# Kernel tuning notes

Hardware: AMD Instinct MI355X
Metric: run time of the kernel (lower is better)

Reference implementation:

```python
import jax, jax.numpy as jnp
import numpy as np

B, S, HID, HEADS = 8, 1024, 1024, 16
DK = HID // HEADS


def setup_inputs() -> dict:
    key = jax.random.key(0)
    ks = jax.random.split(key, 6)
    scale = 1.0 / np.sqrt(HID)
    return {
        "q": jax.random.normal(ks[0], (B, S, HID), jnp.float32),
        "k": jax.random.normal(ks[1], (B, S, HID), jnp.float32),
        "v": jax.random.normal(ks[2], (B, S, HID), jnp.float32),
        "Wq": jax.random.normal(ks[3], (HID, HID), jnp.float32) * scale,
        "Wk": jax.random.normal(ks[4], (HID, HID), jnp.float32) * scale,
        "Wv": jax.random.normal(ks[5], (HID, HID), jnp.float32) * scale,
        "mask": 1,
    }


def _split_heads(x):
    # [B, S, HID] -> [B, HEADS, S, DK]
    b, s, _ = x.shape
    return x.reshape(b, s, HEADS, DK).transpose(0, 2, 1, 3)


def reference(q, k, v, Wq, Wk, Wv, mask):
    # torch nn.Linear: y = x @ W.T (no bias)
    qh = _split_heads(q @ Wq.T)
    kh = _split_heads(k @ Wk.T)
    vh = _split_heads(v @ Wv.T)

    scores = jnp.einsum("bhqd,bhkd->bhqk", qh, kh) / jnp.sqrt(jnp.asarray(DK, qh.dtype))
    scores = jax.nn.softmax(scores, axis=-1)
    if mask:
        # original zeroes entries where row > col AFTER softmax (keeps upper triangle)
        tri = jnp.triu(jnp.ones((S, S), scores.dtype))
        scores = scores * tri
        # original then transposes the (masked) score matrix before applying to V
        scores = scores.transpose(0, 1, 3, 2)
    out = jnp.einsum("bhqk,bhkd->bhqd", scores, vh)
    # [B, HEADS, S, DK] -> [B, S, HID]
    return out.transpose(0, 2, 1, 3).reshape(q.shape[0], -1, HID)
```

## Files before the change

### kernel.cpp

```cpp
#include <hip/hip_runtime.h>
#include <math.h>

#define B 8
#define S 1024
#define HID 1024
#define HEADS 16
#define DK 64

typedef unsigned short u16;
typedef unsigned int u32;
typedef _Float16 f16;
typedef __attribute__((ext_vector_type(8))) _Float16 half8;
typedef __attribute__((ext_vector_type(4))) _Float16 half4;
typedef __attribute__((ext_vector_type(2))) _Float16 half2;
typedef __attribute__((ext_vector_type(2))) __fp16 fp16x2;
typedef __attribute__((ext_vector_type(4))) float f32x4;

#define GLL16(G, L)                                                         \
    __builtin_amdgcn_global_load_lds(                                       \
        (const __attribute__((address_space(1))) u32*)(G),                  \
        (__attribute__((address_space(3))) u32*)(L), 16, 0, 0)

__device__ __forceinline__ float exp_s(float c) {
#if __has_builtin(__builtin_amdgcn_exp2f)
    return __builtin_amdgcn_exp2f(c);
#else
    return exp2f(c);
#endif
}

__global__ __launch_bounds__(256) void cast_all(
    const float* __restrict__ q, const float* __restrict__ k,
    const float* __restrict__ v, const float* __restrict__ Wq,
    const float* __restrict__ Wk, const float* __restrict__ Wv,
    f16* __restrict__ oq, f16* __restrict__ ok, f16* __restrict__ ov,
    f16* __restrict__ owq, f16* __restrict__ owk, f16* __restrict__ owv) {
    const size_t SZ = (size_t)B * S * HID;
    const size_t WZ = (size_t)HID * HID;
    size_t e = ((size_t)blockIdx.x * 256 + threadIdx.x) * 8;
    const float* src;
    f16* dst;
    if (e < SZ)               { src = q + e;               dst = oq + e; }
    else if (e < 2 * SZ)      { src = k + (e - SZ);        dst = ok + (e - SZ); }
    else if (e < 3 * SZ)      { src = v + (e - 2 * SZ);    dst = ov + (e - 2 * SZ); }
    else if (e < 3 * SZ + WZ) { src = Wq + (e - 3 * SZ);   dst = owq + (e - 3 * SZ); }
    else if (e < 3 * SZ + 2 * WZ) { src = Wk + (e - 3 * SZ - WZ); dst = owk + (e - 3 * SZ - WZ); }
    else                      { src = Wv + (e - 3 * SZ - 2 * WZ); dst = owv + (e - 3 * SZ - 2 * WZ); }
    f32x4 a = *(const f32x4*)src;
    f32x4 b = *(const f32x4*)(src + 4);
    half8 h;
    h[0] = (f16)a[0]; h[1] = (f16)a[1]; h[2] = (f16)a[2]; h[3] = (f16)a[3];
    h[4] = (f16)b[0]; h[5] = (f16)b[1]; h[6] = (f16)b[2]; h[7] = (f16)b[3];
    *(half8*)dst = h;
}

__global__ __launch_bounds__(256) void proj_mfma_b(
    const f16* __restrict__ Xq, const f16* __restrict__ Xk,
    const f16* __restrict__ Xv, const f16* __restrict__ Wq,
    const f16* __restrict__ Wk, const f16* __restrict__ Wv,
    f16* __restrict__ Qb, f16* __restrict__ Kb, f16* __restrict__ Vt) {
    const int L = blockIdx.x;
    const int xcd = L & 7;
    const int w8 = L >> 3;
    const int cx = w8 & 7;
    const int g = xcd * 24 + (w8 >> 3);
    const int z = g % 3;
    const int ytile = g / 3;

    const f16* __restrict__ X = (z == 0) ? Xq : (z == 1) ? Xk : Xv;
    const f16* __restrict__ W = (z == 0) ? Wq : (z == 1) ? Wk : Wv;

    __shared__ u16 As[128 * 32];
    __shared__ u16 Bs[128 * 32];
    const int tid = threadIdx.x;
    const int wv = tid >> 6, ln = tid & 63;
    const int lr = ln & 15, quad = ln >> 4;
    const int wm = wv >> 1, wn = wv & 1;
    const int row0 = ytile * 128, col0 = cx * 128;

    const int srow = tid >> 2;
    const int sch = tid & 3;

    f32x4 acc[4][4];
    #pragma unroll
    for (int i = 0; i < 4; ++i)
        #pragma unroll
        for (int j = 0; j < 4; ++j) acc[i][j] = (f32x4){0.f, 0.f, 0.f, 0.f};

    for (int k0 = 0; k0 < HID; k0 += 32) {
        #pragma unroll
        for (int p = 0; p < 2; ++p) {
            int r = p * 64 + srow;
            int csw = sch ^ ((r >> 1) & 3);
            GLL16(X + (size_t)(row0 + r) * HID + k0 + csw * 8, As + p * 2048 + tid * 8);
            GLL16(W + (size_t)(col0 + r) * HID + k0 + csw * 8, Bs + p * 2048 + tid * 8);
        }
        __syncthreads();
        half8 a[4], b[4];
        #pragma unroll
        for (int mi = 0; mi < 4; ++mi) {
            int r = wm * 64 + mi * 16 + lr;
            a[mi] = *(const half8*)(As + r * 32 + ((quad ^ ((r >> 1) & 3)) * 8));
        }
        #pragma unroll
        for (int ni = 0; ni < 4; ++ni) {
            int r = wn * 64 + ni * 16 + lr;
            b[ni] = *(const half8*)(Bs + r * 32 + ((quad ^ ((r >> 1) & 3)) * 8));
        }
        #pragma unroll
        for (int mi = 0; mi < 4; ++mi)
            #pragma unroll
            for (int ni = 0; ni < 4; ++ni)
                acc[mi][ni] = __builtin_amdgcn_mfma_f32_16x16x32_f16(
                    a[mi], b[ni], acc[mi][ni], 0, 0, 0);
        __syncthreads();
    }

    if (z < 2) {
        f16* __restrict__ Y = (z == 0) ? Qb : Kb;
        const float sc = (z == 0) ? 0.18033688f : 1.0f;
        #pragma unroll
        for (int mi = 0; mi < 4; ++mi) {
            int m = row0 + wm * 64 + mi * 16 + quad * 4;
            #pragma unroll
            for (int ni = 0; ni < 4; ++ni) {
                int n = col0 + wn * 64 + ni * 16 + lr;
                #pragma unroll
                for (int r = 0; r < 4; ++r)
                    Y[(size_t)(m + r) * HID + n] = (f16)(acc[mi][ni][r] * sc);
            }
        }
    } else {
        #pragma unroll
        for (int mi = 0; mi < 4; ++mi) {
            int m = row0 + wm * 64 + mi * 16 + quad * 4;
            int bb = m >> 10, s = m & 1023;
            #pragma unroll
            for (int ni = 0; ni < 4; ++ni) {
                int n = col0 + wn * 64 + ni * 16 + lr;
                half4 h4;
                #pragma unroll
                for (int r = 0; r < 4; ++r) h4[r] = (f16)acc[mi][ni][r];
                *(half4*)(Vt + ((size_t)(bb * 16 + (n >> 6)) * 64 + (n & 63)) * S + s) = h4;
            }
        }
    }
}

__global__ __launch_bounds__(256) void stats_mfma(const f16* __restrict__ Q,
                                                  const f16* __restrict__ K,
                                                  f16* __restrict__ Vt) {
    const int bh = blockIdx.x, jt = blockIdx.y;
    const int b = bh >> 4, h = bh & 15;
    const int tid = threadIdx.x;
    const int wv = tid >> 6, ln = tid & 63;
    const int lr = ln & 15, quad = ln >> 4;
    __shared__ u16 Ks[2][64 * 64];
    __shared__ float rlL[128];

    auto stageK = [&](int bufi, int i0v) {
        #pragma unroll
        for (int p = 0; p < 2; ++p) {
            int r = p * 32 + (tid >> 3);
            int csw = (tid & 7) ^ (r & 7);
            GLL16(K + (size_t)(b * S + i0v + r) * HID + h * 64 + csw * 8,
                  Ks[bufi] + p * 2048 + tid * 8);
        }
    };

    stageK(0, 0);

    half8 aq[2][2];
    #pragma unroll
    for (int jsub = 0; jsub < 2; ++jsub) {
        const int j = jt * 128 + wv * 32 + jsub * 16 + lr;
        const f16* qrow = Q + (size_t)(b * S + j) * HID + h * 64;
        aq[jsub][0] = *(const half8*)(qrow + quad * 8);
        aq[jsub][1] = *(const half8*)(qrow + 32 + quad * 8);
    }

    float sl[2][4] = {};

    for (int t = 0; t < S / 64; ++t) {
        __syncthreads();
        if (t + 1 < S / 64) stageK((t + 1) & 1, (t + 1) * 64);
        const u16* Kst = Ks[t & 1];
        #pragma unroll
        for (int isub = 0; isub < 4; ++isub) {
            int il = isub * 16 + lr;
            half8 bk0 = *(const half8*)(Kst + il * 64 + (((0 + quad) ^ (il & 7)) * 8));
            half8 bk1 = *(const half8*)(Kst + il * 64 + (((4 + quad) ^ (il & 7)) * 8));
            #pragma unroll
            for (int jsub = 0; jsub < 2; ++jsub) {
                f32x4 c = {0.f, 0.f, 0.f, 0.f};
                c = __builtin_amdgcn_mfma_f32_16x16x32_f16(aq[jsub][0], bk0, c, 0, 0, 0);
                c = __builtin_amdgcn_mfma_f32_16x16x32_f16(aq[jsub][1], bk1, c, 0, 0, 0);
                #pragma unroll
                for (int r = 0; r < 4; ++r) sl[jsub][r] += exp_s(c[r]);
            }
        }
    }

    #pragma unroll
    for (int jsub = 0; jsub < 2; ++jsub)
        #pragma unroll
        for (int r = 0; r < 4; ++r) {
            float v = sl[jsub][r];
            v += __shfl_xor(v, 1, 64);
            v += __shfl_xor(v, 2, 64);
            v += __shfl_xor(v, 4, 64);
            v += __shfl_xor(v, 8, 64);
            if (lr == 0) rlL[wv * 32 + jsub * 16 + quad * 4 + r] = 1.0f / v;
        }
    __syncthreads();

    {
        const int d = tid >> 2, lc = (tid & 3) * 8;
        f16* vrow = Vt + (size_t)(bh * 64 + d) * S + jt * 128;
        #pragma unroll
        for (int g = 0; g < 4; ++g) {
            const int c0 = g * 32 + lc;
            half8 hv = *(half8*)(vrow + c0);
            #pragma unroll
            for (int e = 0; e < 8; ++e)
                hv[e] = (f16)((float)hv[e] * rlL[c0 + e]);
            *(half8*)(vrow + c0) = hv;
        }
    }
}

__global__ __launch_bounds__(256) void apply_mfma(const f16* __restrict__ Q,
                                                  const f16* __restrict__ K,
                                                  const f16* __restrict__ Vt,
                                                  float* __restrict__ out) {
    const int bh = blockIdx.x;
    const int it2 = (gridDim.y - 1) - blockIdx.y;
    const int b = bh >> 4, h = bh & 15;
    const int tid = threadIdx.x;
    const int wv = tid >> 6, ln = tid & 63;
    const int lr = ln & 15, quad = ln >> 4;
    const int i0b = it2 * 128;
    const int i0w = i0b + wv * 32;

    __shared__ u16 Qs[2][64 * 64];
    __shared__ u16 Vts[2][64 * 64];

    auto stageQV = [&](int bufi, int j0v) {
        #pragma unroll
        for (int p = 0; p < 2; ++p) {
            int r = p * 32 + (tid >> 3);
            int csw = (tid & 7) ^ (r & 7);
            GLL16(Q + (size_t)(b * S + j0v + r) * HID + h * 64 + csw * 8,
                  Qs[bufi] + p * 2048 + tid * 8);
        }
        #pragma unroll
        for (int p = 0; p < 2; ++p) {
            int d = p * 32 + (tid >> 3);
            int csw = (tid & 7) ^ (d & 7);
            GLL16(Vt + (size_t)(bh * 64 + d) * S + j0v + csw * 8,
                  Vts[bufi] + p * 2048 + tid * 8);
        }
    };

    stageQV(0, 0);

    half8 bk[2][2];
    #pragma unroll
    for (int isub = 0; isub < 2; ++isub) {
        int i = i0w + isub * 16 + lr;
        #pragma unroll
        for (int kf = 0; kf < 2; ++kf)
            bk[isub][kf] = *(const half8*)(K + (size_t)(b * S + i) * HID + h * 64 +
                                           kf * 32 + quad * 8);
    }

    f32x4 acc[4][2];
    #pragma unroll
    for (int nt = 0; nt < 4; ++nt)
        #pragma unroll
        for (int isub = 0; isub < 2; ++isub) acc[nt][isub] = (f32x4){0.f, 0.f, 0.f, 0.f};

    const int nch = 2 * it2 + 2;
    for (int jc = 0; jc < nch; ++jc) {
        const int j0 = jc * 64;
        __syncthreads();
        if (jc + 1 < nch) stageQV((jc + 1) & 1, j0 + 64);
        const u16* Qsc = Qs[jc & 1];
        const u16* Vsc = Vts[jc & 1];

        #pragma unroll
        for (int jsub = 0; jsub < 4; ++jsub) {
            const int jbase = j0 + jsub * 16;
            if (jbase > i0w + 31) break;

            const int jl = jsub * 16 + lr;
            half8 aq0 = *(const half8*)(Qsc + jl * 64 + (((0 + quad) ^ (jl & 7)) * 8));
            half8 aq1 = *(const half8*)(Qsc + jl * 64 + (((4 + quad) ^ (jl & 7)) * 8));
            half4 av[4];
            #pragma unroll
            for (int nt = 0; nt < 4; ++nt) {
                int d = nt * 16 + lr;
                int ch = (jsub * 2 + (quad >> 1)) ^ (d & 7);
                av[nt] = *(const half4*)(Vsc + d * 64 + ch * 8 + (quad & 1) * 4);
            }

            #pragma unroll
            for (int isub = 0; isub < 2; ++isub) {
                const int ib = i0w + isub * 16;
                if (jbase > ib + 15) continue;
                f32x4 c = {0.f, 0.f, 0.f, 0.f};
                c = __builtin_amdgcn_mfma_f32_16x16x32_f16(aq0, bk[isub][0], c, 0, 0, 0);
                c = __builtin_amdgcn_mfma_f32_16x16x32_f16(aq1, bk[isub][1], c, 0, 0, 0);
                float w0 = exp_s(c[0]), w1 = exp_s(c[1]);
                float w2 = exp_s(c[2]), w3 = exp_s(c[3]);
                if (jbase + 15 > ib) {
                    const int i_col = ib + lr;
                    const int jq = jbase + quad * 4;
                    if (jq + 0 > i_col) w0 = 0.f;
                    if (jq + 1 > i_col) w1 = 0.f;
                    if (jq + 2 > i_col) w2 = 0.f;
                    if (jq + 3 > i_col) w3 = 0.f;
                }
                fp16x2 q0 = __builtin_amdgcn_cvt_pkrtz(w0, w1);
                fp16x2 q1 = __builtin_amdgcn_cvt_pkrtz(w2, w3);
                half2 p0 = __builtin_bit_cast(half2, q0);
                half2 p1 = __builtin_bit_cast(half2, q1);
                half4 bw;
                bw[0] = p0[0]; bw[1] = p0[1]; bw[2] = p1[0]; bw[3] = p1[1];
                #pragma unroll
                for (int nt = 0; nt < 4; ++nt)
                    acc[nt][isub] = __builtin_amdgcn_mfma_f32_16x16x16f16(
                        av[nt], bw, acc[nt][isub], 0, 0, 0);
            }
        }
    }

    #pragma unroll
    for (int isub = 0; isub < 2; ++isub) {
        int i = i0w + isub * 16 + lr;
        #pragma unroll
        for (int nt = 0; nt < 4; ++nt)
            *(f32x4*)(out + (size_t)(b * S + i) * HID + h * 64 + nt * 16 + quad * 4) =
                acc[nt][isub];
    }
}

extern "C" void kernel_launch(void* const* d_in, const int* in_sizes, int n_in,
                              void* d_out, int out_size, void* d_ws, size_t ws_size,
                              hipStream_t stream) {
    const float* q  = (const float*)d_in[0];
    const float* k  = (const float*)d_in[1];
    const float* v  = (const float*)d_in[2];
    const float* Wq = (const float*)d_in[3];
    const float* Wk = (const float*)d_in[4];
    const float* Wv = (const float*)d_in[5];

    const size_t SZ = (size_t)B * S * HID;
    const size_t WZ = (size_t)HID * HID;

    f16* xq = (f16*)d_out;
    f16* xk = xq + SZ;

    char* p = (char*)d_ws;
    f16* xv = (f16*)p;      p += SZ * 2;
    f16* wq = (f16*)p;      p += WZ * 2;
    f16* wk = (f16*)p;      p += WZ * 2;
    f16* wv_ = (f16*)p;     p += WZ * 2;
    f16* Qb = (f16*)p;      p += SZ * 2;
    f16* Kb = (f16*)p;      p += SZ * 2;
    f16* Vt = (f16*)p;      p += SZ * 2;

    float* out = (float*)d_out;

    const int ncast = (int)((3 * SZ + 3 * WZ) / 8 / 256);
    cast_all<<<ncast, 256, 0, stream>>>(q, k, v, Wq, Wk, Wv,
                                        xq, xk, xv, wq, wk, wv_);

    proj_mfma_b<<<1536, 256, 0, stream>>>(xq, xk, xv, wq, wk, wv_, Qb, Kb, Vt);

    stats_mfma<<<dim3(B * HEADS, S / 128), 256, 0, stream>>>(Qb, Kb, Vt);
    apply_mfma<<<dim3(B * HEADS, S / 128), 256, 0, stream>>>(Qb, Kb, Vt, out);
}
```

Measured before the change: 285.3 us.

## Rework projection GEMM into triple-buffered 256x128 tile pipeline with 8 waves

The Q/K/V projection kernel moves from a 128x128 tile with a single-stage K=32 loop to a 256x128 tile with 512 threads and a K=64 step. Three LDS buffers let global-to-LDS loads for later K steps run while the current step computes, with explicit vmcnt and lgkmcnt waits. Barriers and s_setprio interleave LDS reads with MFMA bursts, and the workgroup-to-XCD mapping changes. The aim is to hide load latency and raise MFMA utilization. In exchange the kernel uses about 144KB of LDS, which limits it to one block per CU, and depends on hand-written wait counts being correct.

```diff
diff --git a/kernel.cpp b/kernel.cpp
--- a/kernel.cpp
+++ b/kernel.cpp
@@ -20,6 +20,8 @@
     __builtin_amdgcn_global_load_lds(                                       \
         (const __attribute__((address_space(1))) u32*)(G),                  \
         (__attribute__((address_space(3))) u32*)(L), 16, 0, 0)
+
+#define MF32(a, b, c) __builtin_amdgcn_mfma_f32_16x16x32_f16((a), (b), (c), 0, 0, 0)
 
 __device__ __forceinline__ float exp_s(float c) {
 #if __has_builtin(__builtin_amdgcn_exp2f)
@@ -54,32 +56,47 @@
     *(half8*)dst = h;
 }
 
-__global__ __launch_bounds__(256) void proj_mfma_b(
+__global__ __launch_bounds__(512, 2) void proj_mfma_b(
     const f16* __restrict__ Xq, const f16* __restrict__ Xk,
     const f16* __restrict__ Xv, const f16* __restrict__ Wq,
     const f16* __restrict__ Wk, const f16* __restrict__ Wv,
     f16* __restrict__ Qb, f16* __restrict__ Kb, f16* __restrict__ Vt) {
     const int L = blockIdx.x;
-    const int xcd = L & 7;
-    const int w8 = L >> 3;
-    const int cx = w8 & 7;
-    const int g = xcd * 24 + (w8 >> 3);
-    const int z = g % 3;
-    const int ytile = g / 3;
+    const int wg = (L & 7) * 96 + (L >> 3);
+    const int z = wg >> 8;
+    const int rm = wg & 255;
+    const int ytile = rm >> 3;
+    const int cx = rm & 7;
 
     const f16* __restrict__ X = (z == 0) ? Xq : (z == 1) ? Xk : Xv;
     const f16* __restrict__ W = (z == 0) ? Wq : (z == 1) ? Wk : Wv;
-
-    __shared__ u16 As[128 * 32];
-    __shared__ u16 Bs[128 * 32];
+    const int row0 = ytile * 256, col0 = cx * 128;
+
+    __shared__ u16 As[3][256 * 64];
+    __shared__ u16 Bs[3][128 * 64];
+
     const int tid = threadIdx.x;
     const int wv = tid >> 6, ln = tid & 63;
     const int lr = ln & 15, quad = ln >> 4;
     const int wm = wv >> 1, wn = wv & 1;
-    const int row0 = ytile * 128, col0 = cx * 128;
-
-    const int srow = tid >> 2;
-    const int sch = tid & 3;
+    const int rr = tid >> 3, ch = tid & 7;
+
+    auto stage = [&](int kt, int bi) {
+        const f16* Xb = X + (size_t)row0 * HID + kt * 64;
+        const f16* Wb = W + (size_t)col0 * HID + kt * 64;
+        #pragma unroll
+        for (int p = 0; p < 4; ++p) {
+            int row = p * 64 + rr;
+            GLL16(Xb + (size_t)row * HID + ((ch ^ (row & 7)) * 8),
+                  &As[bi][p * 4096 + tid * 8]);
+        }
+        #pragma unroll
+        for (int p = 0; p < 2; ++p) {
+            int row = p * 64 + rr;
+            GLL16(Wb + (size_t)row * HID + ((ch ^ (row & 7)) * 8),
+                  &Bs[bi][p * 4096 + tid * 8]);
+        }
+    };
 
     f32x4 acc[4][4];
     #pragma unroll
@@ -87,33 +104,77 @@
         #pragma unroll
         for (int j = 0; j < 4; ++j) acc[i][j] = (f32x4){0.f, 0.f, 0.f, 0.f};
 
-    for (int k0 = 0; k0 < HID; k0 += 32) {
-        #pragma unroll
-        for (int p = 0; p < 2; ++p) {
-            int r = p * 64 + srow;
-            int csw = sch ^ ((r >> 1) & 3);
-            GLL16(X + (size_t)(row0 + r) * HID + k0 + csw * 8, As + p * 2048 + tid * 8);
-            GLL16(W + (size_t)(col0 + r) * HID + k0 + csw * 8, Bs + p * 2048 + tid * 8);
-        }
-        __syncthreads();
-        half8 a[4], b[4];
-        #pragma unroll
-        for (int mi = 0; mi < 4; ++mi) {
-            int r = wm * 64 + mi * 16 + lr;
-            a[mi] = *(const half8*)(As + r * 32 + ((quad ^ ((r >> 1) & 3)) * 8));
-        }
-        #pragma unroll
-        for (int ni = 0; ni < 4; ++ni) {
-            int r = wn * 64 + ni * 16 + lr;
-            b[ni] = *(const half8*)(Bs + r * 32 + ((quad ^ ((r >> 1) & 3)) * 8));
-        }
-        #pragma unroll
-        for (int mi = 0; mi < 4; ++mi)
-            #pragma unroll
-            for (int ni = 0; ni < 4; ++ni)
-                acc[mi][ni] = __builtin_amdgcn_mfma_f32_16x16x32_f16(
-                    a[mi], b[ni], acc[mi][ni], 0, 0, 0);
-        __syncthreads();
+    stage(0, 0);
+    stage(1, 1);
+    asm volatile("s_waitcnt vmcnt(6)" ::: "memory");
+    __builtin_amdgcn_s_barrier();
+
+    int bi = 0, sbi = 2;
+    #pragma unroll
+    for (int u = 0; u < 16; ++u) {
+        const u16* A = As[bi];
+        const u16* Bh = Bs[bi];
+        auto rdA = [&](int mi, int ks) -> half8 {
+            int row = wm * 64 + mi * 16 + lr;
+            int pc = (ks * 4 + quad) ^ (row & 7);
+            return *(const half8*)(A + row * 64 + pc * 8);
+        };
+        auto rdB = [&](int ni, int ks) -> half8 {
+            int row = wn * 64 + ni * 16 + lr;
+            int pc = (ks * 4 + quad) ^ (row & 7);
+            return *(const half8*)(Bh + row * 64 + pc * 8);
+        };
+
+        if (u < 14) stage(u + 2, sbi);
+        half8 a00 = rdA(0, 0), a01 = rdA(0, 1), a10 = rdA(1, 0), a11 = rdA(1, 1);
+        half8 b00 = rdB(0, 0), b01 = rdB(0, 1), b10 = rdB(1, 0), b11 = rdB(1, 1);
+        __builtin_amdgcn_s_barrier();
+        asm volatile("s_waitcnt lgkmcnt(0)" ::: "memory");
+        __builtin_amdgcn_s_setprio(1);
+        acc[0][0] = MF32(a00, b00, acc[0][0]); acc[0][0] = MF32(a01, b01, acc[0][0]);
+        acc[0][1] = MF32(a00, b10, acc[0][1]); acc[0][1] = MF32(a01, b11, acc[0][1]);
+        acc[1][0] = MF32(a10, b00, acc[1][0]); acc[1][0] = MF32(a11, b01, acc[1][0]);
+        acc[1][1] = MF32(a10, b10, acc[1][1]); acc[1][1] = MF32(a11, b11, acc[1][1]);
+        __builtin_amdgcn_s_setprio(0);
+        __builtin_amdgcn_s_barrier();
+
+        half8 b20 = rdB(2, 0), b21 = rdB(2, 1), b30 = rdB(3, 0), b31 = rdB(3, 1);
+        __builtin_amdgcn_s_barrier();
+        asm volatile("s_waitcnt lgkmcnt(0)" ::: "memory");
+        __builtin_amdgcn_s_setprio(1);
+        acc[0][2] = MF32(a00, b20, acc[0][2]); acc[0][2] = MF32(a01, b21, acc[0][2]);
+        acc[0][3] = MF32(a00, b30, acc[0][3]); acc[0][3] = MF32(a01, b31, acc[0][3]);
+        acc[1][2] = MF32(a10, b20, acc[1][2]); acc[1][2] = MF32(a11, b21, acc[1][2]);
+        acc[1][3] = MF32(a10, b30, acc[1][3]); acc[1][3] = MF32(a11, b31, acc[1][3]);
+        __builtin_amdgcn_s_setprio(0);
+        __builtin_amdgcn_s_barrier();
+
+        half8 a20 = rdA(2, 0), a21 = rdA(2, 1), a30 = rdA(3, 0), a31 = rdA(3, 1);
+        __builtin_amdgcn_s_barrier();
+        asm volatile("s_waitcnt lgkmcnt(0)" ::: "memory");
+        __builtin_amdgcn_s_setprio(1);
+        acc[2][2] = MF32(a20, b20, acc[2][2]); acc[2][2] = MF32(a21, b21, acc[2][2]);
+        acc[2][3] = MF32(a20, b30, acc[2][3]); acc[2][3] = MF32(a21, b31, acc[2][3]);
+        acc[3][2] = MF32(a30, b20, acc[3][2]); acc[3][2] = MF32(a31, b21, acc[3][2]);
+        acc[3][3] = MF32(a30, b30, acc[3][3]); acc[3][3] = MF32(a31, b31, acc[3][3]);
+        __builtin_amdgcn_s_setprio(0);
+        __builtin_amdgcn_s_barrier();
+
+        __builtin_amdgcn_s_setprio(1);
+        acc[2][0] = MF32(a20, b00, acc[2][0]); acc[2][0] = MF32(a21, b01, acc[2][0]);
+        acc[2][1] = MF32(a20, b10, acc[2][1]); acc[2][1] = MF32(a21, b11, acc[2][1]);
+        acc[3][0] = MF32(a30, b00, acc[3][0]); acc[3][0] = MF32(a31, b01, acc[3][0]);
+        acc[3][1] = MF32(a30, b10, acc[3][1]); acc[3][1] = MF32(a31, b11, acc[3][1]);
+        __builtin_amdgcn_s_setprio(0);
+        if (u < 14) {
+            asm volatile("s_waitcnt vmcnt(6)" ::: "memory");
+        } else if (u == 14) {
+            asm volatile("s_waitcnt vmcnt(0)" ::: "memory");
+        }
+        __builtin_amdgcn_s_barrier();
+
+        bi = (bi + 1 == 3) ? 0 : bi + 1;
+        sbi = (sbi + 1 == 3) ? 0 : sbi + 1;
     }
 
     if (z < 2) {
@@ -376,7 +437,7 @@
     cast_all<<<ncast, 256, 0, stream>>>(q, k, v, Wq, Wk, Wv,
                                         xq, xk, xv, wq, wk, wv_);
 
-    proj_mfma_b<<<1536, 256, 0, stream>>>(xq, xk, xv, wq, wk, wv_, Qb, Kb, Vt);
+    proj_mfma_b<<<768, 512, 0, stream>>>(xq, xk, xv, wq, wk, wv_, Qb, Kb, Vt);
 
     stats_mfma<<<dim3(B * HEADS, S / 128), 256, 0, stream>>>(Qb, Kb, Vt);
     apply_mfma<<<dim3(B * HEADS, S / 128), 256, 0, stream>>>(Qb, Kb, Vt, out);
```

New measurement: 280.0 us. No clear change (-1.9%).

## Fuse fp32-to-fp16 activation cast into projection GEMM with double-buffered LDS

Applied to the files above, without the earlier changes.

Drops the separate cast pass over q/k/v. The projection kernel now loads fp32 activations into registers, converts them to fp16 and writes them into a swizzled LDS tile. The LDS tiles are double-buffered so the next k-slice loads overlap the current MFMA work, and only the weights are still pre-cast. This saves writing and re-reading 3x fp16 activation copies. In exchange the GEMM reads twice the activation bytes per tile and holds more registers, and each iteration ends with a vmcnt(0) wait.

```diff
diff --git a/kernel.cpp b/kernel.cpp
--- a/kernel.cpp
+++ b/kernel.cpp
@@ -21,6 +21,8 @@
         (const __attribute__((address_space(1))) u32*)(G),                  \
         (__attribute__((address_space(3))) u32*)(L), 16, 0, 0)
 
+#define MF32(a, b, c) __builtin_amdgcn_mfma_f32_16x16x32_f16((a), (b), (c), 0, 0, 0)
+
 __device__ __forceinline__ float exp_s(float c) {
 #if __has_builtin(__builtin_amdgcn_exp2f)
     return __builtin_amdgcn_exp2f(c);
@@ -29,23 +31,17 @@
 #endif
 }
 
-__global__ __launch_bounds__(256) void cast_all(
-    const float* __restrict__ q, const float* __restrict__ k,
-    const float* __restrict__ v, const float* __restrict__ Wq,
-    const float* __restrict__ Wk, const float* __restrict__ Wv,
-    f16* __restrict__ oq, f16* __restrict__ ok, f16* __restrict__ ov,
+__global__ __launch_bounds__(256) void cast_w(
+    const float* __restrict__ Wq, const float* __restrict__ Wk,
+    const float* __restrict__ Wv,
     f16* __restrict__ owq, f16* __restrict__ owk, f16* __restrict__ owv) {
-    const size_t SZ = (size_t)B * S * HID;
     const size_t WZ = (size_t)HID * HID;
     size_t e = ((size_t)blockIdx.x * 256 + threadIdx.x) * 8;
     const float* src;
     f16* dst;
-    if (e < SZ)               { src = q + e;               dst = oq + e; }
-    else if (e < 2 * SZ)      { src = k + (e - SZ);        dst = ok + (e - SZ); }
-    else if (e < 3 * SZ)      { src = v + (e - 2 * SZ);    dst = ov + (e - 2 * SZ); }
-    else if (e < 3 * SZ + WZ) { src = Wq + (e - 3 * SZ);   dst = owq + (e - 3 * SZ); }
-    else if (e < 3 * SZ + 2 * WZ) { src = Wk + (e - 3 * SZ - WZ); dst = owk + (e - 3 * SZ - WZ); }
-    else                      { src = Wv + (e - 3 * SZ - 2 * WZ); dst = owv + (e - 3 * SZ - 2 * WZ); }
+    if (e < WZ)          { src = Wq + e;          dst = owq + e; }
+    else if (e < 2 * WZ) { src = Wk + (e - WZ);   dst = owk + (e - WZ); }
+    else                 { src = Wv + (e - 2*WZ); dst = owv + (e - 2*WZ); }
     f32x4 a = *(const f32x4*)src;
     f32x4 b = *(const f32x4*)(src + 4);
     half8 h;
@@ -55,8 +51,8 @@
 }
 
 __global__ __launch_bounds__(256) void proj_mfma_b(
-    const f16* __restrict__ Xq, const f16* __restrict__ Xk,
-    const f16* __restrict__ Xv, const f16* __restrict__ Wq,
+    const float* __restrict__ Xq, const float* __restrict__ Xk,
+    const float* __restrict__ Xv, const f16* __restrict__ Wq,
     const f16* __restrict__ Wk, const f16* __restrict__ Wv,
     f16* __restrict__ Qb, f16* __restrict__ Kb, f16* __restrict__ Vt) {
     const int L = blockIdx.x;
@@ -67,19 +63,20 @@
     const int z = g % 3;
     const int ytile = g / 3;
 
-    const f16* __restrict__ X = (z == 0) ? Xq : (z == 1) ? Xk : Xv;
+    const float* __restrict__ X = (z == 0) ? Xq : (z == 1) ? Xk : Xv;
     const f16* __restrict__ W = (z == 0) ? Wq : (z == 1) ? Wk : Wv;
 
-    __shared__ u16 As[128 * 32];
-    __shared__ u16 Bs[128 * 32];
+    __shared__ u16 As[2][128 * 32];
+    __shared__ u16 Bs[2][128 * 32];
     const int tid = threadIdx.x;
     const int wv = tid >> 6, ln = tid & 63;
     const int lr = ln & 15, quad = ln >> 4;
     const int wm = wv >> 1, wn = wv & 1;
     const int row0 = ytile * 128, col0 = cx * 128;
 
-    const int srow = tid >> 2;
-    const int sch = tid & 3;
+    const int arow = tid >> 1, ahalf = tid & 1;
+    const float* Xrow = X + (size_t)(row0 + arow) * HID + ahalf * 16;
+    const int brow = tid >> 2, bsch = tid & 3;
 
     f32x4 acc[4][4];
     #pragma unroll
@@ -87,32 +84,65 @@
         #pragma unroll
         for (int j = 0; j < 4; ++j) acc[i][j] = (f32x4){0.f, 0.f, 0.f, 0.f};
 
-    for (int k0 = 0; k0 < HID; k0 += 32) {
+    f32x4 ar[4];
+    auto loadA = [&](int k0) {
+        #pragma unroll
+        for (int j = 0; j < 4; ++j)
+            ar[j] = *(const f32x4*)(Xrow + k0 + j * 4);
+    };
+    auto writeA = [&](int bufi) {
+        half8 h0, h1;
+        h0[0] = (f16)ar[0][0]; h0[1] = (f16)ar[0][1]; h0[2] = (f16)ar[0][2]; h0[3] = (f16)ar[0][3];
+        h0[4] = (f16)ar[1][0]; h0[5] = (f16)ar[1][1]; h0[6] = (f16)ar[1][2]; h0[7] = (f16)ar[1][3];
+        h1[0] = (f16)ar[2][0]; h1[1] = (f16)ar[2][1]; h1[2] = (f16)ar[2][2]; h1[3] = (f16)ar[2][3];
+        h1[4] = (f16)ar[3][0]; h1[5] = (f16)ar[3][1]; h1[6] = (f16)ar[3][2]; h1[7] = (f16)ar[3][3];
+        const int sw = (arow >> 1) & 3;
+        *(half8*)(&As[bufi][arow * 32 + ((ahalf * 2 + 0) ^ sw) * 8]) = h0;
+        *(half8*)(&As[bufi][arow * 32 + ((ahalf * 2 + 1) ^ sw) * 8]) = h1;
+    };
+    auto stageB = [&](int k0, int bufi) {
         #pragma unroll
         for (int p = 0; p < 2; ++p) {
-            int r = p * 64 + srow;
-            int csw = sch ^ ((r >> 1) & 3);
-            GLL16(X + (size_t)(row0 + r) * HID + k0 + csw * 8, As + p * 2048 + tid * 8);
-            GLL16(W + (size_t)(col0 + r) * HID + k0 + csw * 8, Bs + p * 2048 + tid * 8);
-        }
-        __syncthreads();
+            int r = p * 64 + brow;
+            int csw = bsch ^ ((r >> 1) & 3);
+            GLL16(W + (size_t)(col0 + r) * HID + k0 + csw * 8,
+                  &Bs[bufi][p * 2048 + tid * 8]);
+        }
+    };
+
+    loadA(0);
+    stageB(0, 0);
+    asm volatile("s_waitcnt vmcnt(0)" ::: "memory");
+    writeA(0);
+    __syncthreads();
+
+    #pragma unroll 2
+    for (int t = 0; t < 32; ++t) {
+        const int cur = t & 1, nxt = cur ^ 1;
+        if (t < 31) {
+            loadA((t + 1) * 32);
+            stageB((t + 1) * 32, nxt);
+        }
         half8 a[4], b[4];
         #pragma unroll
         for (int mi = 0; mi < 4; ++mi) {
             int r = wm * 64 + mi * 16 + lr;
-            a[mi] = *(const half8*)(As + r * 32 + ((quad ^ ((r >> 1) & 3)) * 8));
+            a[mi] = *(const half8*)(&As[cur][r * 32 + ((quad ^ ((r >> 1) & 3)) * 8)]);
         }
         #pragma unroll
         for (int ni = 0; ni < 4; ++ni) {
             int r = wn * 64 + ni * 16 + lr;
-            b[ni] = *(const half8*)(Bs + r * 32 + ((quad ^ ((r >> 1) & 3)) * 8));
+            b[ni] = *(const half8*)(&Bs[cur][r * 32 + ((quad ^ ((r >> 1) & 3)) * 8)]);
         }
         #pragma unroll
         for (int mi = 0; mi < 4; ++mi)
             #pragma unroll
             for (int ni = 0; ni < 4; ++ni)
-                acc[mi][ni] = __builtin_amdgcn_mfma_f32_16x16x32_f16(
-                    a[mi], b[ni], acc[mi][ni], 0, 0, 0);
+                acc[mi][ni] = MF32(a[mi], b[ni], acc[mi][ni]);
+        if (t < 31) {
+            asm volatile("s_waitcnt vmcnt(0)" ::: "memory");
+            writeA(nxt);
+        }
         __syncthreads();
     }
 
@@ -358,11 +388,7 @@
     const size_t SZ = (size_t)B * S * HID;
     const size_t WZ = (size_t)HID * HID;
 
-    f16* xq = (f16*)d_out;
-    f16* xk = xq + SZ;
-
     char* p = (char*)d_ws;
-    f16* xv = (f16*)p;      p += SZ * 2;
     f16* wq = (f16*)p;      p += WZ * 2;
     f16* wk = (f16*)p;      p += WZ * 2;
     f16* wv_ = (f16*)p;     p += WZ * 2;
@@ -372,11 +398,10 @@
 
     float* out = (float*)d_out;
 
-    const int ncast = (int)((3 * SZ + 3 * WZ) / 8 / 256);
-    cast_all<<<ncast, 256, 0, stream>>>(q, k, v, Wq, Wk, Wv,
-                                        xq, xk, xv, wq, wk, wv_);
-
-    proj_mfma_b<<<1536, 256, 0, stream>>>(xq, xk, xv, wq, wk, wv_, Qb, Kb, Vt);
+    const int ncast = (int)(3 * WZ / 8 / 256);
+    cast_w<<<ncast, 256, 0, stream>>>(Wq, Wk, Wv, wq, wk, wv_);
+
+    proj_mfma_b<<<1536, 256, 0, stream>>>(q, k, v, wq, wk, wv_, Qb, Kb, Vt);
 
     stats_mfma<<<dim3(B * HEADS, S / 128), 256, 0, stream>>>(Qb, Kb, Vt);
     apply_mfma<<<dim3(B * HEADS, S / 128), 256, 0, stream>>>(Qb, Kb, Vt, out);
```

New measurement: 317.1 us. 1.11x slower.

## Replace LDS double-buffered staging with direct global loads in stats and apply kernels

Applied to the files above, without the earlier changes.

Both the stats and apply attention kernels stop staging K, Q and transposed V tiles into shared memory with async global-to-LDS copies and barriers. Each wave now reads its MFMA operands straight from global memory, relying on L1/L2 caching. This removes the __syncthreads barriers and LDS traffic, and lets the apply kernel loop per 16-row chunk with per-wave early exit. The cost is redundant global and cache reads across the four waves, plus exposed load latency with no explicit prefetch.

```diff
diff --git a/kernel.cpp b/kernel.cpp
--- a/kernel.cpp
+++ b/kernel.cpp
@@ -155,20 +155,7 @@
     const int tid = threadIdx.x;
     const int wv = tid >> 6, ln = tid & 63;
     const int lr = ln & 15, quad = ln >> 4;
-    __shared__ u16 Ks[2][64 * 64];
     __shared__ float rlL[128];
-
-    auto stageK = [&](int bufi, int i0v) {
-        #pragma unroll
-        for (int p = 0; p < 2; ++p) {
-            int r = p * 32 + (tid >> 3);
-            int csw = (tid & 7) ^ (r & 7);
-            GLL16(K + (size_t)(b * S + i0v + r) * HID + h * 64 + csw * 8,
-                  Ks[bufi] + p * 2048 + tid * 8);
-        }
-    };
-
-    stageK(0, 0);
 
     half8 aq[2][2];
     #pragma unroll
@@ -181,15 +168,13 @@
 
     float sl[2][4] = {};
 
-    for (int t = 0; t < S / 64; ++t) {
-        __syncthreads();
-        if (t + 1 < S / 64) stageK((t + 1) & 1, (t + 1) * 64);
-        const u16* Kst = Ks[t & 1];
+    for (int i0 = 0; i0 < S; i0 += 64) {
         #pragma unroll
         for (int isub = 0; isub < 4; ++isub) {
-            int il = isub * 16 + lr;
-            half8 bk0 = *(const half8*)(Kst + il * 64 + (((0 + quad) ^ (il & 7)) * 8));
-            half8 bk1 = *(const half8*)(Kst + il * 64 + (((4 + quad) ^ (il & 7)) * 8));
+            const int i = i0 + isub * 16 + lr;
+            const f16* krow = K + (size_t)(b * S + i) * HID + h * 64;
+            half8 bk0 = *(const half8*)(krow + quad * 8);
+            half8 bk1 = *(const half8*)(krow + 32 + quad * 8);
             #pragma unroll
             for (int jsub = 0; jsub < 2; ++jsub) {
                 f32x4 c = {0.f, 0.f, 0.f, 0.f};
@@ -242,28 +227,6 @@
     const int i0b = it2 * 128;
     const int i0w = i0b + wv * 32;
 
-    __shared__ u16 Qs[2][64 * 64];
-    __shared__ u16 Vts[2][64 * 64];
-
-    auto stageQV = [&](int bufi, int j0v) {
-        #pragma unroll
-        for (int p = 0; p < 2; ++p) {
-            int r = p * 32 + (tid >> 3);
-            int csw = (tid & 7) ^ (r & 7);
-            GLL16(Q + (size_t)(b * S + j0v + r) * HID + h * 64 + csw * 8,
-                  Qs[bufi] + p * 2048 + tid * 8);
-        }
-        #pragma unroll
-        for (int p = 0; p < 2; ++p) {
-            int d = p * 32 + (tid >> 3);
-            int csw = (tid & 7) ^ (d & 7);
-            GLL16(Vt + (size_t)(bh * 64 + d) * S + j0v + csw * 8,
-                  Vts[bufi] + p * 2048 + tid * 8);
-        }
-    };
-
-    stageQV(0, 0);
-
     half8 bk[2][2];
     #pragma unroll
     for (int isub = 0; isub < 2; ++isub) {
@@ -280,58 +243,47 @@
         #pragma unroll
         for (int isub = 0; isub < 2; ++isub) acc[nt][isub] = (f32x4){0.f, 0.f, 0.f, 0.f};
 
-    const int nch = 2 * it2 + 2;
-    for (int jc = 0; jc < nch; ++jc) {
-        const int j0 = jc * 64;
-        __syncthreads();
-        if (jc + 1 < nch) stageQV((jc + 1) & 1, j0 + 64);
-        const u16* Qsc = Qs[jc & 1];
-        const u16* Vsc = Vts[jc & 1];
-
-        #pragma unroll
-        for (int jsub = 0; jsub < 4; ++jsub) {
-            const int jbase = j0 + jsub * 16;
-            if (jbase > i0w + 31) break;
-
-            const int jl = jsub * 16 + lr;
-            half8 aq0 = *(const half8*)(Qsc + jl * 64 + (((0 + quad) ^ (jl & 7)) * 8));
-            half8 aq1 = *(const half8*)(Qsc + jl * 64 + (((4 + quad) ^ (jl & 7)) * 8));
-            half4 av[4];
-            #pragma unroll
-            for (int nt = 0; nt < 4; ++nt) {
-                int d = nt * 16 + lr;
-                int ch = (jsub * 2 + (quad >> 1)) ^ (d & 7);
-                av[nt] = *(const half4*)(Vsc + d * 64 + ch * 8 + (quad & 1) * 4);
+    const int nj16 = (i0w + 32) >> 4;
+    for (int js = 0; js < nj16; ++js) {
+        const int jbase = js * 16;
+
+        const int jl = jbase + lr;
+        const f16* qrow = Q + (size_t)(b * S + jl) * HID + h * 64;
+        half8 aq0 = *(const half8*)(qrow + quad * 8);
+        half8 aq1 = *(const half8*)(qrow + 32 + quad * 8);
+        half4 av[4];
+        #pragma unroll
+        for (int nt = 0; nt < 4; ++nt)
+            av[nt] = *(const half4*)(Vt + (size_t)(bh * 64 + nt * 16 + lr) * S +
+                                     jbase + quad * 4);
+
+        #pragma unroll
+        for (int isub = 0; isub < 2; ++isub) {
+            const int ib = i0w + isub * 16;
+            if (jbase > ib + 15) continue;
+            f32x4 c = {0.f, 0.f, 0.f, 0.f};
+            c = __builtin_amdgcn_mfma_f32_16x16x32_f16(aq0, bk[isub][0], c, 0, 0, 0);
+            c = __builtin_amdgcn_mfma_f32_16x16x32_f16(aq1, bk[isub][1], c, 0, 0, 0);
+            float w0 = exp_s(c[0]), w1 = exp_s(c[1]);
+            float w2 = exp_s(c[2]), w3 = exp_s(c[3]);
+            if (jbase + 15 > ib) {
+                const int i_col = ib + lr;
+                const int jq = jbase + quad * 4;
+                if (jq + 0 > i_col) w0 = 0.f;
+                if (jq + 1 > i_col) w1 = 0.f;
+                if (jq + 2 > i_col) w2 = 0.f;
+                if (jq + 3 > i_col) w3 = 0.f;
             }
-
-            #pragma unroll
-            for (int isub = 0; isub < 2; ++isub) {
-                const int ib = i0w + isub * 16;
-                if (jbase > ib + 15) continue;
-                f32x4 c = {0.f, 0.f, 0.f, 0.f};
-                c = __builtin_amdgcn_mfma_f32_16x16x32_f16(aq0, bk[isub][0], c, 0, 0, 0);
-                c = __builtin_amdgcn_mfma_f32_16x16x32_f16(aq1, bk[isub][1], c, 0, 0, 0);
-                float w0 = exp_s(c[0]), w1 = exp_s(c[1]);
-                float w2 = exp_s(c[2]), w3 = exp_s(c[3]);
-                if (jbase + 15 > ib) {
-                    const int i_col = ib + lr;
-                    const int jq = jbase + quad * 4;
-                    if (jq + 0 > i_col) w0 = 0.f;
-                    if (jq + 1 > i_col) w1 = 0.f;
-                    if (jq + 2 > i_col) w2 = 0.f;
-                    if (jq + 3 > i_col) w3 = 0.f;
-                }
-                fp16x2 q0 = __builtin_amdgcn_cvt_pkrtz(w0, w1);
-                fp16x2 q1 = __builtin_amdgcn_cvt_pkrtz(w2, w3);
-                half2 p0 = __builtin_bit_cast(half2, q0);
-                half2 p1 = __builtin_bit_cast(half2, q1);
-                half4 bw;
-                bw[0] = p0[0]; bw[1] = p0[1]; bw[2] = p1[0]; bw[3] = p1[1];
-                #pragma unroll
-                for (int nt = 0; nt < 4; ++nt)
-                    acc[nt][isub] = __builtin_amdgcn_mfma_f32_16x16x16f16(
-                        av[nt], bw, acc[nt][isub], 0, 0, 0);
-            }
+            fp16x2 q0 = __builtin_amdgcn_cvt_pkrtz(w0, w1);
+            fp16x2 q1 = __builtin_amdgcn_cvt_pkrtz(w2, w3);
+            half2 p0 = __builtin_bit_cast(half2, q0);
+            half2 p1 = __builtin_bit_cast(half2, q1);
+            half4 bw;
+            bw[0] = p0[0]; bw[1] = p0[1]; bw[2] = p1[0]; bw[3] = p1[1];
+            #pragma unroll
+            for (int nt = 0; nt < 4; ++nt)
+                acc[nt][isub] = __builtin_amdgcn_mfma_f32_16x16x16f16(
+                    av[nt], bw, acc[nt][isub], 0, 0, 0);
         }
     }
 
```

Result: slower. 378.1 us (+32.5%).
